# Kernel tuning notes

Measured on AMD Instinct MI355X. Metric: run time of the kernel, lower is better.

## Reference

```python
import jax, jax.numpy as jnp
import numpy as np


def setup_inputs() -> dict:
    key = jax.random.key(0)
    ks = jax.random.split(key, 7)
    C, IC, H, W, B = 512, 256, 64, 64, 8
    N = H * W
    return {
        "x": jax.random.normal(ks[0], (B, C, H, W), dtype=jnp.float32),
        "w_phi": jax.random.normal(ks[1], (IC, C), dtype=jnp.float32) * 0.02,
        "w_theta": jax.random.normal(ks[2], (IC, C), dtype=jnp.float32) * 0.02,
        "w_g": jax.random.normal(ks[3], (IC, C), dtype=jnp.float32) * 0.02,
        "w_mask": jax.random.normal(ks[4], (C, IC), dtype=jnp.float32) * 0.02,
        "pos_embedding": jax.random.normal(ks[5], (1, N, N), dtype=jnp.float32),
        "pos_embedding_decoder": jax.random.normal(ks[6], (1, IC, H, W), dtype=jnp.float32),
    }


def reference(x, w_phi, w_theta, w_g, w_mask, pos_embedding, pos_embedding_decoder):
    b, c, h, w = x.shape
    n = h * w
    xf = x.reshape(b, c, n)  # [b, c, n]
    # 1x1 convs as channel matmuls
    phi = jnp.einsum('oc,bcn->bon', w_phi, xf)      # [b, ic, n]
    theta = jnp.einsum('oc,bcn->bon', w_theta, xf)  # [b, ic, n]
    g = jnp.einsum('oc,bcn->bon', w_g, xf) + pos_embedding_decoder.reshape(1, -1, n)
    g = jnp.swapaxes(g, 1, 2)  # [b, n, ic]
    # attention logits: theta^T @ phi -> [b, n_theta, n_phi], plus learned pos bias
    attn = jnp.einsum('bci,bcj->bij', theta, phi) + pos_embedding
    # NOTE: original softmax is over dim=1 (the theta/query axis), non-standard
    attn = jax.nn.softmax(attn, axis=1)
    y = jnp.einsum('bij,bjc->bic', attn, g)  # [b, n, ic]
    y = jnp.swapaxes(y, 1, 2).reshape(b, -1, n)  # [b, ic, n]
    mask = jnp.einsum('oc,bcn->bon', w_mask, y).reshape(b, c, h, w)
    return mask + x
```

## Files before the change

kernel.cpp:

```cpp
#include <hip/hip_runtime.h>

typedef short bf8 __attribute__((ext_vector_type(8)));
typedef float f32x4 __attribute__((ext_vector_type(4)));
typedef unsigned short us4 __attribute__((ext_vector_type(4)));
typedef unsigned short us8 __attribute__((ext_vector_type(8)));

#define DEVI __device__ __forceinline__

constexpr int NB = 8, NC = 512, NIC = 256, NS = 4096;

constexpr size_t OFF_XT  = 0;
constexpr size_t OFF_RS  = 0;
constexpr size_t OFF_TP  = 33554432;
constexpr size_t OFF_POS = 67108864;
constexpr size_t OFF_G   = 100663296;
constexpr size_t OFF_G2  = 117440512;
constexpr size_t OFF_Y   = 134217728;
constexpr size_t OFF_WTP = 150994944;
constexpr size_t OFF_WG  = 151519232;
constexpr size_t OFF_WM  = 151781376;

DEVI unsigned short f2bf(float f){
  unsigned u = __float_as_uint(f);
  u += 0x7fffu + ((u >> 16) & 1u);
  return (unsigned short)(u >> 16);
}
DEVI float bf2f(unsigned short b){ return __uint_as_float(((unsigned)b) << 16); }

DEVI void gld16(const void* g, void* l){
  __builtin_amdgcn_global_load_lds((const __attribute__((address_space(1))) unsigned int*)g,
                                   (__attribute__((address_space(3))) unsigned int*)l, 16, 0, 0);
}

DEVI void stageT(unsigned short* dst, const unsigned short* src, int ld, int wid, int lane){
  int rl = lane >> 3;
  int ce = ((lane & 7) << 3) ^ (rl << 3);
#pragma unroll
  for (int it = 0; it < 4; ++it){
    int q = wid + it * 4;
    gld16(src + (size_t)(q * 8 + rl) * ld + ce, dst + q * 512);
  }
}

DEVI void zero44(f32x4 (&a)[4][4]){
  f32x4 z = {0.f, 0.f, 0.f, 0.f};
#pragma unroll
  for (int i = 0; i < 4; ++i)
#pragma unroll
    for (int j = 0; j < 4; ++j) a[i][j] = z;
}

template<int NK64>
DEVI void gemm128v(const unsigned short* Ag, int lda, const unsigned short* Bg, int ldb,
                   unsigned short (&As)[2][8192], unsigned short (&Bs)[2][8192],
                   f32x4 (&acc)[4][4], int wid, int lane)
{
  const int wr = wid >> 1, wc = wid & 1;
  stageT(As[0], Ag, lda, wid, lane);
  stageT(Bs[0], Bg, ldb, wid, lane);
  __syncthreads();
  for (int kt = 0; kt < NK64; ++kt){
    int cur = kt & 1;
    if (kt + 1 < NK64){
      stageT(As[cur ^ 1], Ag + (kt + 1) * 64, lda, wid, lane);
      stageT(Bs[cur ^ 1], Bg + (kt + 1) * 64, ldb, wid, lane);
    }
    bf8 a[2][4], b[2][4];
#pragma unroll
    for (int ks = 0; ks < 2; ++ks){
      int cb = ks * 64 + ((lane >> 4) << 4);
#pragma unroll
      for (int f = 0; f < 4; ++f){
        int rA = wr * 64 + f * 16 + (lane & 15);
        a[ks][f] = *(const bf8*)((char*)As[cur] + rA * 128 + (cb ^ ((rA & 7) << 4)));
        int rB = wc * 64 + f * 16 + (lane & 15);
        b[ks][f] = *(const bf8*)((char*)Bs[cur] + rB * 128 + (cb ^ ((rB & 7) << 4)));
      }
    }
    __builtin_amdgcn_s_setprio(1);
#pragma unroll
    for (int ks = 0; ks < 2; ++ks)
#pragma unroll
      for (int i = 0; i < 4; ++i)
#pragma unroll
        for (int j = 0; j < 4; ++j)
          acc[i][j] = __builtin_amdgcn_mfma_f32_16x16x32_bf16(a[ks][i], b[ks][j], acc[i][j], 0, 0, 0);
    __builtin_amdgcn_s_setprio(0);
    __syncthreads();
  }
}


__global__ void k_prep(const float* wphi, const float* wtheta, const float* wgf, const float* wmf,
                       unsigned short* wtp, unsigned short* wgb, unsigned short* wmb){
  int idx = (blockIdx.x * 256 + threadIdx.x) * 4;
  const float* src; unsigned short* dst;
  if (idx < 131072)      { src = wphi + idx;            dst = wtp + idx; }
  else if (idx < 262144) { src = wtheta + (idx - 131072); dst = wtp + idx; }
  else if (idx < 393216) { src = wgf + (idx - 262144);  dst = wgb + (idx - 262144); }
  else                   { src = wmf + (idx - 393216);  dst = wmb + (idx - 393216); }
  f32x4 v = *(const f32x4*)src;
  us4 o;
#pragma unroll
  for (int r = 0; r < 4; ++r) o[r] = f2bf(v[r]);
  *(us4*)dst = o;
}

__global__ void k_pos(const float* pos, unsigned short* posb){
  size_t base = ((size_t)blockIdx.x * 256 + threadIdx.x) * 8;
  f32x4 v0 = *(const f32x4*)&pos[base];
  f32x4 v1 = *(const f32x4*)&pos[base + 4];
  us8 o;
#pragma unroll
  for (int r = 0; r < 4; ++r){ o[r] = f2bf(v0[r]); o[r + 4] = f2bf(v1[r]); }
  *(us8*)&posb[base] = o;
}

__global__ void k_xt(const float* x, unsigned short* xT){
  int b = blockIdx.z, ct = blockIdx.y, nt = blockIdx.x;
  __shared__ float t[64][65];
  int tid = threadIdx.x;
  int c0 = ct * 64, n0 = nt * 64;
  const float* xp = x + (size_t)b * NC * NS;
#pragma unroll
  for (int it = 0; it < 16; ++it){
    int idx = it * 256 + tid; int r = idx >> 6, cc = idx & 63;
    t[r][cc] = xp[(size_t)(c0 + r) * NS + n0 + cc];
  }
  __syncthreads();
  unsigned short* xo = xT + (size_t)b * NS * NC;
#pragma unroll
  for (int it = 0; it < 16; ++it){
    int idx = it * 256 + tid; int r = idx >> 6, cc = idx & 63;
    xo[(size_t)(n0 + r) * NC + c0 + cc] = f2bf(t[cc][r]);
  }
}


__global__ __launch_bounds__(256, 2) void k_tp(const unsigned short* wtp, const unsigned short* xT,
                                               unsigned short* tp){
  int b = blockIdx.z, ot = blockIdx.y, nt = blockIdx.x;
  int tid = threadIdx.x, wid = tid >> 6, lane = tid & 63, wr = wid >> 1, wc = wid & 1;
  __shared__ unsigned short As[2][8192], Bs[2][8192];
  f32x4 acc[4][4]; zero44(acc);
  gemm128v<8>(wtp + (size_t)(ot * 128) * 512, 512,
              xT + ((size_t)b * NS + nt * 128) * 512, 512, As, Bs, acc, wid, lane);
  unsigned short* out = tp + (size_t)b * NS * 512;
#pragma unroll
  for (int fr = 0; fr < 4; ++fr)
#pragma unroll
    for (int fc = 0; fc < 4; ++fc){
      int o0 = ot * 128 + wr * 64 + fr * 16 + ((lane >> 4) << 2);
      int n  = nt * 128 + wc * 64 + fc * 16 + (lane & 15);
      us4 v;
#pragma unroll
      for (int r = 0; r < 4; ++r) v[r] = f2bf(acc[fr][fc][r]);
      *(us4*)&out[(size_t)n * 512 + o0] = v;
    }
}

__global__ __launch_bounds__(256, 2) void k_g(const unsigned short* xT, const unsigned short* wgb,
                                              const float* pdec, unsigned short* gb){
  int b = blockIdx.z, ot = blockIdx.y, nt = blockIdx.x;
  int tid = threadIdx.x, wid = tid >> 6, lane = tid & 63, wr = wid >> 1, wc = wid & 1;
  __shared__ unsigned short As[2][8192], Bs[2][8192];
  f32x4 acc[4][4]; zero44(acc);
  gemm128v<8>(xT + ((size_t)b * NS + nt * 128) * 512, 512,
              wgb + (size_t)(ot * 128) * 512, 512, As, Bs, acc, wid, lane);
#pragma unroll
  for (int fr = 0; fr < 4; ++fr)
#pragma unroll
    for (int fc = 0; fc < 4; ++fc){
      int n0 = nt * 128 + wr * 64 + fr * 16 + ((lane >> 4) << 2);
      int o  = ot * 128 + wc * 64 + fc * 16 + (lane & 15);
      f32x4 pd = *(const f32x4*)&pdec[(size_t)o * NS + n0];
      us4 v;
#pragma unroll
      for (int r = 0; r < 4; ++r) v[r] = f2bf(acc[fr][fc][r] + pd[r]);
      *(us4*)&gb[((size_t)b * NIC + o) * NS + n0] = v;
    }
}

__global__ __launch_bounds__(256, 2) void k_stats(const unsigned short* __restrict__ tp,
                                                  const unsigned short* __restrict__ posb,
                                                  float* __restrict__ rs){
  int bid = blockIdx.x;
  int b = bid & 7, jb0 = (bid >> 3) * 64;
  int tid = threadIdx.x, wid = tid >> 6, lane = tid & 63;
  int p = wid >> 1, q = wid & 1, h = lane >> 4, l15 = lane & 15;
  __shared__ unsigned short Ath[4][128 * 64];
  __shared__ float red[64];
  const unsigned short* tpb = tp + (size_t)b * NS * 512;

  bf8 bphi[8][2];
#pragma unroll
  for (int kb = 0; kb < 8; ++kb)
#pragma unroll
    for (int frj = 0; frj < 2; ++frj)
      bphi[kb][frj] = *(const bf8*)&tpb[(size_t)(jb0 + p * 32 + frj * 16 + l15) * 512
                                        + kb * 32 + h * 8];

  float sacc[2][4];
#pragma unroll
  for (int a = 0; a < 2; ++a)
#pragma unroll
    for (int r = 0; r < 4; ++r) sacc[a][r] = 0.f;

  stageT(Ath[0], tpb + 256, 512, wid, lane);
  stageT(Ath[1], tpb + 256 + 64, 512, wid, lane);

  for (int it = 0; it < 32; ++it){
    int i0t = it * 128;
    const unsigned short* thBase = tpb + (size_t)i0t * 512 + 256;
    const unsigned short* thNext = tpb + (size_t)(it < 31 ? i0t + 128 : i0t) * 512 + 256;
    us4 pv[2][4];
#pragma unroll
    for (int frj = 0; frj < 2; ++frj)
#pragma unroll
      for (int fci = 0; fci < 4; ++fci){
        int iG = i0t + q * 64 + fci * 16 + l15;
        int jG = jb0 + p * 32 + frj * 16 + h * 4;
        pv[frj][fci] = *(const us4*)&posb[(size_t)iG * NS + jG];
      }
    f32x4 lacc[2][4];
    {
      f32x4 z = {0.f, 0.f, 0.f, 0.f};
#pragma unroll
      for (int a = 0; a < 2; ++a)
#pragma unroll
        for (int c = 0; c < 4; ++c) lacc[a][c] = z;
    }
#pragma unroll
    for (int ph = 0; ph < 4; ++ph){
      const unsigned short* ssrc = (ph < 2) ? thBase + (ph + 2) * 64 : thNext + (ph - 2) * 64;
      stageT(Ath[(ph + 2) & 3], ssrc, 512, wid, lane);
      if (ph < 2) asm volatile("s_waitcnt vmcnt(16)" ::: "memory");
      else        asm volatile("s_waitcnt vmcnt(8)"  ::: "memory");
      __builtin_amdgcn_s_barrier();
      __builtin_amdgcn_sched_barrier(0);
#pragma unroll
      for (int ks = 0; ks < 2; ++ks){
        bf8 tfr[4];
#pragma unroll
        for (int fci = 0; fci < 4; ++fci){
          int rI = q * 64 + fci * 16 + l15;
          int cbyte = (ks * 64 + (h << 4)) ^ ((rI & 7) << 4);
          tfr[fci] = *(const bf8*)((char*)Ath[ph] + rI * 128 + cbyte);
        }
        __builtin_amdgcn_s_setprio(1);
#pragma unroll
        for (int frj = 0; frj < 2; ++frj)
#pragma unroll
          for (int fci = 0; fci < 4; ++fci)
            lacc[frj][fci] = __builtin_amdgcn_mfma_f32_16x16x32_bf16(bphi[ph * 2 + ks][frj], tfr[fci],
                                                                     lacc[frj][fci], 0, 0, 0);
        __builtin_amdgcn_s_setprio(0);
      }
    }
#pragma unroll
    for (int frj = 0; frj < 2; ++frj)
#pragma unroll
      for (int fci = 0; fci < 4; ++fci)
#pragma unroll
        for (int r = 0; r < 4; ++r)
          sacc[frj][r] += __expf(lacc[frj][fci][r] + bf2f(pv[frj][fci][r]));
  }
#pragma unroll
  for (int m = 1; m <= 8; m <<= 1)
#pragma unroll
    for (int frj = 0; frj < 2; ++frj)
#pragma unroll
      for (int r = 0; r < 4; ++r)
        sacc[frj][r] += __shfl_xor(sacc[frj][r], m, 64);
  if (q == 0 && l15 == 0){
#pragma unroll
    for (int frj = 0; frj < 2; ++frj)
#pragma unroll
      for (int r = 0; r < 4; ++r)
        red[p * 32 + frj * 16 + h * 4 + r] = sacc[frj][r];
  }
  __syncthreads();
  if (q == 1 && l15 == 0){
#pragma unroll
    for (int frj = 0; frj < 2; ++frj)
#pragma unroll
      for (int r = 0; r < 4; ++r){
        int jl = p * 32 + frj * 16 + h * 4 + r;
        float s = sacc[frj][r] + red[jl];
        rs[(size_t)b * NS + jb0 + jl] = 1.f / s;
      }
  }
}

__global__ void k_sg(const unsigned short* gb, const float* rs, unsigned short* g2){
  size_t base = ((size_t)blockIdx.x * 256 + threadIdx.x) * 8;
  int b = (int)(base / ((size_t)NIC * NS));
  int j0 = (int)(base % NS);
  const float* rsb = rs + (size_t)b * NS + j0;
  f32x4 r0 = *(const f32x4*)&rsb[0];
  f32x4 r1 = *(const f32x4*)&rsb[4];
  us8 gv = *(const us8*)&gb[base];
  us8 o;
#pragma unroll
  for (int r = 0; r < 4; ++r){
    o[r]     = f2bf(bf2f(gv[r])     * r0[r]);
    o[r + 4] = f2bf(bf2f(gv[r + 4]) * r1[r]);
  }
  *(us8*)&g2[base] = o;
}

__global__ __launch_bounds__(256, 2) void k_y(const unsigned short* __restrict__ tp,
                                              const unsigned short* __restrict__ posb,
                                              const unsigned short* __restrict__ g2,
                                              unsigned short* __restrict__ yb){
  int bid = blockIdx.x;
  int b = bid & 7, i0 = (bid >> 3) * 64;
  int tid = threadIdx.x, wid = tid >> 6, lane = tid & 63;
  int p = wid >> 1, q = wid & 1;
  __shared__ unsigned short Aph[4][128 * 64];
  __shared__ unsigned short El[64 * 128];
  const unsigned short* tpb = tp + (size_t)b * NS * 512;

  bf8 btr[8][2];
#pragma unroll
  for (int kb = 0; kb < 8; ++kb)
#pragma unroll
    for (int fc = 0; fc < 2; ++fc)
      btr[kb][fc] = *(const bf8*)&tpb[(size_t)(i0 + p * 32 + fc * 16 + (lane & 15)) * 512
                                      + 256 + kb * 32 + (lane >> 4) * 8];

  f32x4 yacc[4][4]; zero44(yacc);
  stageT(Aph[0], tpb, 512, wid, lane);
  stageT(Aph[1], tpb + 64, 512, wid, lane);

  const unsigned short* g2b = g2 + (size_t)b * NIC * NS;

  for (int jt = 0; jt < 32; ++jt){
    int j0 = jt * 128;
    const unsigned short* phiBase = tpb + (size_t)j0 * 512;
    const unsigned short* phiNext = tpb + (size_t)(jt < 31 ? j0 + 128 : j0) * 512;
    us4 pv[4][2];
#pragma unroll
    for (int fr = 0; fr < 4; ++fr){
      int jl = q * 64 + fr * 16 + ((lane >> 4) << 2);
#pragma unroll
      for (int fc = 0; fc < 2; ++fc){
        int il = p * 32 + fc * 16 + (lane & 15);
        pv[fr][fc] = *(const us4*)&posb[(size_t)(i0 + il) * NS + j0 + jl];
      }
    }
    f32x4 lacc[4][2];
    {
      f32x4 z = {0.f, 0.f, 0.f, 0.f};
#pragma unroll
      for (int i = 0; i < 4; ++i)
#pragma unroll
        for (int j = 0; j < 2; ++j) lacc[i][j] = z;
    }
#pragma unroll
    for (int ph = 0; ph < 4; ++ph){
      const unsigned short* ssrc = (ph < 2) ? phiBase + (ph + 2) * 64 : phiNext + (ph - 2) * 64;
      stageT(Aph[(ph + 2) & 3], ssrc, 512, wid, lane);
      if (ph < 2) asm volatile("s_waitcnt vmcnt(16)" ::: "memory");
      else        asm volatile("s_waitcnt vmcnt(8)"  ::: "memory");
      __builtin_amdgcn_s_barrier();
      __builtin_amdgcn_sched_barrier(0);
#pragma unroll
      for (int ks = 0; ks < 2; ++ks){
        bf8 a[4];
#pragma unroll
        for (int fr = 0; fr < 4; ++fr){
          int r = q * 64 + fr * 16 + (lane & 15);
          int cbyte = (ks * 64 + ((lane >> 4) << 4)) ^ ((r & 7) << 4);
          a[fr] = *(const bf8*)((char*)Aph[ph] + r * 128 + cbyte);
        }
        __builtin_amdgcn_s_setprio(1);
#pragma unroll
        for (int fr = 0; fr < 4; ++fr)
#pragma unroll
          for (int fc = 0; fc < 2; ++fc)
            lacc[fr][fc] = __builtin_amdgcn_mfma_f32_16x16x32_bf16(a[fr], btr[ph * 2 + ks][fc],
                                                                   lacc[fr][fc], 0, 0, 0);
        __builtin_amdgcn_s_setprio(0);
      }
    }
#pragma unroll
    for (int fr = 0; fr < 4; ++fr)
#pragma unroll
      for (int fc = 0; fc < 2; ++fc){
        int il = p * 32 + fc * 16 + (lane & 15);
        int jl = q * 64 + fr * 16 + ((lane >> 4) << 2);
        us4 ev;
#pragma unroll
        for (int r = 0; r < 4; ++r)
          ev[r] = f2bf(__expf(lacc[fr][fc][r] + bf2f(pv[fr][fc][r])));
        *(us4*)((char*)El + il * 256 + ((jl * 2) ^ ((il & 7) << 4))) = ev;
      }
    __builtin_amdgcn_sched_barrier(0);
    asm volatile("s_waitcnt lgkmcnt(0)" ::: "memory");
    __builtin_amdgcn_s_barrier();
    __builtin_amdgcn_sched_barrier(0);
#pragma unroll
    for (int jk = 0; jk < 4; ++jk){
      bf8 eb[4];
#pragma unroll
      for (int f = 0; f < 4; ++f){
        int ei = f * 16 + (lane & 15);
        int ebt = jk * 64 + ((lane >> 4) << 4);
        eb[f] = *(const bf8*)((char*)El + ei * 256 + (ebt ^ ((ei & 7) << 4)));
      }
      __builtin_amdgcn_s_setprio(1);
#pragma unroll
      for (int cf = 0; cf < 4; ++cf){
        int c = wid * 64 + cf * 16 + (lane & 15);
        bf8 ga = *(const bf8*)&g2b[(size_t)c * NS + j0 + jk * 32 + (lane >> 4) * 8];
#pragma unroll
        for (int f = 0; f < 4; ++f)
          yacc[cf][f] = __builtin_amdgcn_mfma_f32_16x16x32_bf16(ga, eb[f], yacc[cf][f], 0, 0, 0);
      }
      __builtin_amdgcn_s_setprio(0);
    }
  }
  unsigned short* yo = yb + (size_t)b * NS * NIC;
#pragma unroll
  for (int cf = 0; cf < 4; ++cf)
#pragma unroll
    for (int f = 0; f < 4; ++f){
      int c0 = wid * 64 + cf * 16 + ((lane >> 4) << 2);
      int ig = i0 + f * 16 + (lane & 15);
      us4 v;
#pragma unroll
      for (int r = 0; r < 4; ++r) v[r] = f2bf(yacc[cf][f][r]);
      *(us4*)&yo[(size_t)ig * NIC + c0] = v;
    }
}

__global__ __launch_bounds__(256, 2) void k_out(const unsigned short* yb, const unsigned short* wmb,
                                                const float* xg, float* outg){
  int b = blockIdx.z, cot = blockIdx.y, nt = blockIdx.x;
  int tid = threadIdx.x, wid = tid >> 6, lane = tid & 63, wr = wid >> 1, wc = wid & 1;
  __shared__ unsigned short As[2][8192], Bs[2][8192];
  f32x4 acc[4][4]; zero44(acc);
  gemm128v<4>(yb + ((size_t)b * NS + nt * 128) * 256, 256,
              wmb + (size_t)(cot * 128) * 256, 256, As, Bs, acc, wid, lane);
#pragma unroll
  for (int fr = 0; fr < 4; ++fr)
#pragma unroll
    for (int fc = 0; fc < 4; ++fc){
      int n0 = nt * 128 + wr * 64 + fr * 16 + ((lane >> 4) << 2);
      int co = cot * 128 + wc * 64 + fc * 16 + (lane & 15);
      f32x4 xv = *(const f32x4*)&xg[((size_t)b * NC + co) * NS + n0];
      f32x4 ov = acc[fr][fc] + xv;
      *(f32x4*)&outg[((size_t)b * NC + co) * NS + n0] = ov;
    }
}

extern "C" void kernel_launch(void* const* d_in, const int* in_sizes, int n_in,
                              void* d_out, int out_size, void* d_ws, size_t ws_size,
                              hipStream_t stream){
  const float* x      = (const float*)d_in[0];
  const float* wphi   = (const float*)d_in[1];
  const float* wtheta = (const float*)d_in[2];
  const float* wgf    = (const float*)d_in[3];
  const float* wmf    = (const float*)d_in[4];
  const float* pos    = (const float*)d_in[5];
  const float* pdec   = (const float*)d_in[6];
  float* outg = (float*)d_out;
  char* ws = (char*)d_ws;
  unsigned short* xT   = (unsigned short*)(ws + OFF_XT);
  float*          rsv  = (float*)(ws + OFF_RS);
  unsigned short* tp   = (unsigned short*)(ws + OFF_TP);
  unsigned short* posb = (unsigned short*)(ws + OFF_POS);
  unsigned short* gb   = (unsigned short*)(ws + OFF_G);
  unsigned short* g2   = (unsigned short*)(ws + OFF_G2);
  unsigned short* yb   = (unsigned short*)(ws + OFF_Y);
  unsigned short* wtp  = (unsigned short*)(ws + OFF_WTP);
  unsigned short* wgb  = (unsigned short*)(ws + OFF_WG);
  unsigned short* wmb  = (unsigned short*)(ws + OFF_WM);

  k_prep<<<512, 256, 0, stream>>>(wphi, wtheta, wgf, wmf, wtp, wgb, wmb);
  k_pos<<<8192, 256, 0, stream>>>(pos, posb);
  k_xt<<<dim3(64, 8, 8), 256, 0, stream>>>(x, xT);
  k_tp<<<dim3(32, 4, 8), 256, 0, stream>>>(wtp, xT, tp);
  k_g<<<dim3(32, 2, 8), 256, 0, stream>>>(xT, wgb, pdec, gb);
  k_stats<<<512, 256, 0, stream>>>(tp, posb, rsv);
  k_sg<<<4096, 256, 0, stream>>>(gb, rsv, g2);
  k_y<<<512, 256, 0, stream>>>(tp, posb, g2, yb);
  k_out<<<dim3(32, 4, 8), 256, 0, stream>>>(yb, wmb, x, outg);
}
```

Measured before the change: 483.5 us.

## Halve LDS staging tiles in stats and y kernels to raise occupancy to 3

The k_stats and k_y kernels now stage the streamed theta/phi tiles in 32-column K slices instead of 64-column slices. This halves each LDS ring buffer and lets launch_bounds request 3 blocks per CU instead of 2. The ring rotation becomes 8 phases per tile with a single vmcnt(4) wait and a new XOR swizzle for 64-byte rows. The trade-off is twice as many barriers per tile and fewer MFMAs between barriers, plus tighter register budgets under the higher occupancy bound, which may cause spills.

```diff
diff --git a/kernel.cpp b/kernel.cpp
--- a/kernel.cpp
+++ b/kernel.cpp
@@ -39,6 +39,18 @@
   for (int it = 0; it < 4; ++it){
     int q = wid + it * 4;
     gld16(src + (size_t)(q * 8 + rl) * ld + ce, dst + q * 512);
+  }
+}
+
+DEVI void stage32(unsigned short* dst, const unsigned short* src, int ld, int wid, int lane){
+  int rl = lane >> 2;
+  int slot = lane & 3;
+#pragma unroll
+  for (int it = 0; it < 2; ++it){
+    int q = wid + it * 4;
+    int row = q * 16 + rl;
+    int ce = ((slot ^ ((row >> 1) & 3)) << 3);
+    gld16(src + (size_t)row * ld + ce, dst + q * 512);
   }
 }
 
@@ -181,14 +193,14 @@
     }
 }
 
-__global__ __launch_bounds__(256, 2) void k_stats(const unsigned short* __restrict__ tp,
+__global__ __launch_bounds__(256, 3) void k_stats(const unsigned short* __restrict__ tp,
                                                   const unsigned short* __restrict__ posb,
                                                   float* __restrict__ rs){
   int bid = blockIdx.x;
   int b = bid & 7, jb0 = (bid >> 3) * 64;
   int tid = threadIdx.x, wid = tid >> 6, lane = tid & 63;
   int p = wid >> 1, q = wid & 1, h = lane >> 4, l15 = lane & 15;
-  __shared__ unsigned short Ath[4][128 * 64];
+  __shared__ unsigned short Ath[4][4096];
   __shared__ float red[64];
   const unsigned short* tpb = tp + (size_t)b * NS * 512;
 
@@ -206,8 +218,8 @@
 #pragma unroll
     for (int r = 0; r < 4; ++r) sacc[a][r] = 0.f;
 
-  stageT(Ath[0], tpb + 256, 512, wid, lane);
-  stageT(Ath[1], tpb + 256 + 64, 512, wid, lane);
+  stage32(Ath[0], tpb + 256, 512, wid, lane);
+  stage32(Ath[1], tpb + 256 + 32, 512, wid, lane);
 
   for (int it = 0; it < 32; ++it){
     int i0t = it * 128;
@@ -231,31 +243,27 @@
         for (int c = 0; c < 4; ++c) lacc[a][c] = z;
     }
 #pragma unroll
-    for (int ph = 0; ph < 4; ++ph){
-      const unsigned short* ssrc = (ph < 2) ? thBase + (ph + 2) * 64 : thNext + (ph - 2) * 64;
-      stageT(Ath[(ph + 2) & 3], ssrc, 512, wid, lane);
-      if (ph < 2) asm volatile("s_waitcnt vmcnt(16)" ::: "memory");
-      else        asm volatile("s_waitcnt vmcnt(8)"  ::: "memory");
+    for (int ph = 0; ph < 8; ++ph){
+      const unsigned short* ssrc = (ph < 6) ? thBase + (ph + 2) * 32 : thNext + (ph - 6) * 32;
+      stage32(Ath[(ph + 2) & 3], ssrc, 512, wid, lane);
+      asm volatile("s_waitcnt vmcnt(4)" ::: "memory");
       __builtin_amdgcn_s_barrier();
       __builtin_amdgcn_sched_barrier(0);
-#pragma unroll
-      for (int ks = 0; ks < 2; ++ks){
-        bf8 tfr[4];
-#pragma unroll
-        for (int fci = 0; fci < 4; ++fci){
-          int rI = q * 64 + fci * 16 + l15;
-          int cbyte = (ks * 64 + (h << 4)) ^ ((rI & 7) << 4);
-          tfr[fci] = *(const bf8*)((char*)Ath[ph] + rI * 128 + cbyte);
-        }
-        __builtin_amdgcn_s_setprio(1);
-#pragma unroll
-        for (int frj = 0; frj < 2; ++frj)
-#pragma unroll
-          for (int fci = 0; fci < 4; ++fci)
-            lacc[frj][fci] = __builtin_amdgcn_mfma_f32_16x16x32_bf16(bphi[ph * 2 + ks][frj], tfr[fci],
-                                                                     lacc[frj][fci], 0, 0, 0);
-        __builtin_amdgcn_s_setprio(0);
-      }
+      bf8 tfr[4];
+#pragma unroll
+      for (int fci = 0; fci < 4; ++fci){
+        int rI = q * 64 + fci * 16 + l15;
+        int cbyte = ((h ^ ((rI >> 1) & 3)) << 4);
+        tfr[fci] = *(const bf8*)((char*)Ath[ph & 3] + rI * 64 + cbyte);
+      }
+      __builtin_amdgcn_s_setprio(1);
+#pragma unroll
+      for (int frj = 0; frj < 2; ++frj)
+#pragma unroll
+        for (int fci = 0; fci < 4; ++fci)
+          lacc[frj][fci] = __builtin_amdgcn_mfma_f32_16x16x32_bf16(bphi[ph][frj], tfr[fci],
+                                                                   lacc[frj][fci], 0, 0, 0);
+      __builtin_amdgcn_s_setprio(0);
     }
 #pragma unroll
     for (int frj = 0; frj < 2; ++frj)
@@ -309,7 +317,7 @@
   *(us8*)&g2[base] = o;
 }
 
-__global__ __launch_bounds__(256, 2) void k_y(const unsigned short* __restrict__ tp,
+__global__ __launch_bounds__(256, 3) void k_y(const unsigned short* __restrict__ tp,
                                               const unsigned short* __restrict__ posb,
                                               const unsigned short* __restrict__ g2,
                                               unsigned short* __restrict__ yb){
@@ -317,7 +325,7 @@
   int b = bid & 7, i0 = (bid >> 3) * 64;
   int tid = threadIdx.x, wid = tid >> 6, lane = tid & 63;
   int p = wid >> 1, q = wid & 1;
-  __shared__ unsigned short Aph[4][128 * 64];
+  __shared__ unsigned short Aph[4][4096];
   __shared__ unsigned short El[64 * 128];
   const unsigned short* tpb = tp + (size_t)b * NS * 512;
 
@@ -330,8 +338,8 @@
                                       + 256 + kb * 32 + (lane >> 4) * 8];
 
   f32x4 yacc[4][4]; zero44(yacc);
-  stageT(Aph[0], tpb, 512, wid, lane);
-  stageT(Aph[1], tpb + 64, 512, wid, lane);
+  stage32(Aph[0], tpb, 512, wid, lane);
+  stage32(Aph[1], tpb + 32, 512, wid, lane);
 
   const unsigned short* g2b = g2 + (size_t)b * NIC * NS;
 
@@ -358,31 +366,27 @@
         for (int j = 0; j < 2; ++j) lacc[i][j] = z;
     }
 #pragma unroll
-    for (int ph = 0; ph < 4; ++ph){
-      const unsigned short* ssrc = (ph < 2) ? phiBase + (ph + 2) * 64 : phiNext + (ph - 2) * 64;
-      stageT(Aph[(ph + 2) & 3], ssrc, 512, wid, lane);
-      if (ph < 2) asm volatile("s_waitcnt vmcnt(16)" ::: "memory");
-      else        asm volatile("s_waitcnt vmcnt(8)"  ::: "memory");
+    for (int ph = 0; ph < 8; ++ph){
+      const unsigned short* ssrc = (ph < 6) ? phiBase + (ph + 2) * 32 : phiNext + (ph - 6) * 32;
+      stage32(Aph[(ph + 2) & 3], ssrc, 512, wid, lane);
+      asm volatile("s_waitcnt vmcnt(4)" ::: "memory");
       __builtin_amdgcn_s_barrier();
       __builtin_amdgcn_sched_barrier(0);
-#pragma unroll
-      for (int ks = 0; ks < 2; ++ks){
-        bf8 a[4];
-#pragma unroll
-        for (int fr = 0; fr < 4; ++fr){
-          int r = q * 64 + fr * 16 + (lane & 15);
-          int cbyte = (ks * 64 + ((lane >> 4) << 4)) ^ ((r & 7) << 4);
-          a[fr] = *(const bf8*)((char*)Aph[ph] + r * 128 + cbyte);
-        }
-        __builtin_amdgcn_s_setprio(1);
-#pragma unroll
-        for (int fr = 0; fr < 4; ++fr)
-#pragma unroll
-          for (int fc = 0; fc < 2; ++fc)
-            lacc[fr][fc] = __builtin_amdgcn_mfma_f32_16x16x32_bf16(a[fr], btr[ph * 2 + ks][fc],
-                                                                   lacc[fr][fc], 0, 0, 0);
-        __builtin_amdgcn_s_setprio(0);
-      }
+      bf8 a[4];
+#pragma unroll
+      for (int fr = 0; fr < 4; ++fr){
+        int r = q * 64 + fr * 16 + (lane & 15);
+        int cbyte = (((lane >> 4) ^ ((r >> 1) & 3)) << 4);
+        a[fr] = *(const bf8*)((char*)Aph[ph & 3] + r * 64 + cbyte);
+      }
+      __builtin_amdgcn_s_setprio(1);
+#pragma unroll
+      for (int fr = 0; fr < 4; ++fr)
+#pragma unroll
+        for (int fc = 0; fc < 2; ++fc)
+          lacc[fr][fc] = __builtin_amdgcn_mfma_f32_16x16x32_bf16(a[fr], btr[ph][fc],
+                                                                 lacc[fr][fc], 0, 0, 0);
+      __builtin_amdgcn_s_setprio(0);
     }
 #pragma unroll
     for (int fr = 0; fr < 4; ++fr)
```

Result: slower. 829.1 us (+71.5%).

## Materialize exp attention matrix in stats pass and compute y via plain GEMM

Applied to the files above, without the earlier changes.

The stats kernel now optionally writes the exponentiated attention logits as a bf16 matrix E (B x N x N) to workspace. A new GEMM kernel then computes y from E and the row-scaled g, instead of recomputing the logits and exponentials in k_y. This removes the second QK^T recompute and exp pass but writes and reads a 256 MB intermediate. The path runs only when the workspace is large enough, with a fallback to the old path.

```diff
diff --git a/kernel.cpp b/kernel.cpp
--- a/kernel.cpp
+++ b/kernel.cpp
@@ -19,6 +19,8 @@
 constexpr size_t OFF_WTP = 150994944;
 constexpr size_t OFF_WG  = 151519232;
 constexpr size_t OFF_WM  = 151781376;
+constexpr size_t OFF_E   = 152043520;
+constexpr size_t E_END   = OFF_E + (size_t)268435456;
 
 DEVI unsigned short f2bf(float f){
   unsigned u = __float_as_uint(f);
@@ -181,16 +183,19 @@
     }
 }
 
-__global__ __launch_bounds__(256, 2) void k_stats(const unsigned short* __restrict__ tp,
-                                                  const unsigned short* __restrict__ posb,
-                                                  float* __restrict__ rs){
+template<bool SE>
+__global__ __launch_bounds__(256, 2) void k_statsE(const unsigned short* __restrict__ tp,
+                                                   const unsigned short* __restrict__ posb,
+                                                   float* __restrict__ rs,
+                                                   unsigned short* __restrict__ E){
   int bid = blockIdx.x;
   int b = bid & 7, jb0 = (bid >> 3) * 64;
   int tid = threadIdx.x, wid = tid >> 6, lane = tid & 63;
   int p = wid >> 1, q = wid & 1, h = lane >> 4, l15 = lane & 15;
-  __shared__ unsigned short Ath[4][128 * 64];
+  __shared__ unsigned short Ath[4][8192];
   __shared__ float red[64];
   const unsigned short* tpb = tp + (size_t)b * NS * 512;
+  unsigned short* Eb = SE ? (E + (size_t)b * NS * NS) : nullptr;
 
   bf8 bphi[8][2];
 #pragma unroll
@@ -260,10 +265,20 @@
 #pragma unroll
     for (int frj = 0; frj < 2; ++frj)
 #pragma unroll
-      for (int fci = 0; fci < 4; ++fci)
-#pragma unroll
-        for (int r = 0; r < 4; ++r)
-          sacc[frj][r] += __expf(lacc[frj][fci][r] + bf2f(pv[frj][fci][r]));
+      for (int fci = 0; fci < 4; ++fci){
+        us4 ev;
+#pragma unroll
+        for (int r = 0; r < 4; ++r){
+          float e = __expf(lacc[frj][fci][r] + bf2f(pv[frj][fci][r]));
+          sacc[frj][r] += e;
+          if (SE) ev[r] = f2bf(e);
+        }
+        if (SE){
+          int iG = i0t + q * 64 + fci * 16 + l15;
+          int jG = jb0 + p * 32 + frj * 16 + h * 4;
+          *(us4*)&Eb[(size_t)iG * NS + jG] = ev;
+        }
+      }
   }
 #pragma unroll
   for (int m = 1; m <= 8; m <<= 1)
@@ -309,6 +324,29 @@
   *(us8*)&g2[base] = o;
 }
 
+__global__ __launch_bounds__(256, 2) void k_yg(const unsigned short* __restrict__ g2,
+                                               const unsigned short* __restrict__ E,
+                                               unsigned short* __restrict__ yb){
+  int b = blockIdx.z, ct = blockIdx.y, nt = blockIdx.x;
+  int tid = threadIdx.x, wid = tid >> 6, lane = tid & 63, wr = wid >> 1, wc = wid & 1;
+  __shared__ unsigned short As[2][8192], Bs[2][8192];
+  f32x4 acc[4][4]; zero44(acc);
+  gemm128v<64>(g2 + ((size_t)b * NIC + ct * 128) * NS, NS,
+               E + ((size_t)b * NS + nt * 128) * NS, NS, As, Bs, acc, wid, lane);
+  unsigned short* yo = yb + (size_t)b * NS * NIC;
+#pragma unroll
+  for (int fr = 0; fr < 4; ++fr)
+#pragma unroll
+    for (int fc = 0; fc < 4; ++fc){
+      int c0 = ct * 128 + wr * 64 + fr * 16 + ((lane >> 4) << 2);
+      int i  = nt * 128 + wc * 64 + fc * 16 + (lane & 15);
+      us4 v;
+#pragma unroll
+      for (int r = 0; r < 4; ++r) v[r] = f2bf(acc[fr][fc][r]);
+      *(us4*)&yo[(size_t)i * NIC + c0] = v;
+    }
+}
+
 __global__ __launch_bounds__(256, 2) void k_y(const unsigned short* __restrict__ tp,
                                               const unsigned short* __restrict__ posb,
                                               const unsigned short* __restrict__ g2,
@@ -317,7 +355,7 @@
   int b = bid & 7, i0 = (bid >> 3) * 64;
   int tid = threadIdx.x, wid = tid >> 6, lane = tid & 63;
   int p = wid >> 1, q = wid & 1;
-  __shared__ unsigned short Aph[4][128 * 64];
+  __shared__ unsigned short Aph[4][8192];
   __shared__ unsigned short El[64 * 128];
   const unsigned short* tpb = tp + (size_t)b * NS * 512;
 
@@ -477,14 +515,24 @@
   unsigned short* wtp  = (unsigned short*)(ws + OFF_WTP);
   unsigned short* wgb  = (unsigned short*)(ws + OFF_WG);
   unsigned short* wmb  = (unsigned short*)(ws + OFF_WM);
+  unsigned short* Ebuf = (unsigned short*)(ws + OFF_E);
+
+  bool epath = (ws_size >= E_END);
 
   k_prep<<<512, 256, 0, stream>>>(wphi, wtheta, wgf, wmf, wtp, wgb, wmb);
   k_pos<<<8192, 256, 0, stream>>>(pos, posb);
   k_xt<<<dim3(64, 8, 8), 256, 0, stream>>>(x, xT);
   k_tp<<<dim3(32, 4, 8), 256, 0, stream>>>(wtp, xT, tp);
   k_g<<<dim3(32, 2, 8), 256, 0, stream>>>(xT, wgb, pdec, gb);
-  k_stats<<<512, 256, 0, stream>>>(tp, posb, rsv);
-  k_sg<<<4096, 256, 0, stream>>>(gb, rsv, g2);
-  k_y<<<512, 256, 0, stream>>>(tp, posb, g2, yb);
+
+  if (epath){
+    k_statsE<true><<<512, 256, 0, stream>>>(tp, posb, rsv, Ebuf);
+    k_sg<<<4096, 256, 0, stream>>>(gb, rsv, g2);
+    k_yg<<<dim3(32, 2, 8), 256, 0, stream>>>(g2, Ebuf, yb);
+  } else {
+    k_statsE<false><<<512, 256, 0, stream>>>(tp, posb, rsv, nullptr);
+    k_sg<<<4096, 256, 0, stream>>>(gb, rsv, g2);
+    k_y<<<512, 256, 0, stream>>>(tp, posb, g2, yb);
+  }
   k_out<<<dim3(32, 4, 8), 256, 0, stream>>>(yb, wmb, x, outg);
 }
```

Result: no change. 485.8 us (+0.5%).
